# Performance work log

Hardware: AMD Instinct MI355X
Metric: run time of the kernel (lower is better)

Reference implementation:

```python
import jax, jax.numpy as jnp
import numpy as np

HIDDEN = 256
NUM_REL = 6
NUM_BASES = 30
N_NODES = 50000
N_EDGES = 800000


def rgcn_gate_layer(x, src, dst, etype, basis, att, root, bias, gate_w, gate_b):
    # Basis-decomposed relation weights: W_r = sum_b att[r,b] * basis[b]
    N = x.shape[0]
    W = jnp.einsum('rb,bio->rio', att, basis)           # [R, d, d]
    # Transform all nodes under every relation (cheaper than per-edge matmul
    # since N*R < E), then gather the per-edge message.
    xw = jnp.einsum('nd,rde->rne', x, W)                # [R, N, d]
    msg = xw[etype, src]                                # [E, d]
    # Scalar sigmoid gate per edge message
    g = jax.nn.sigmoid(msg @ gate_w + gate_b)           # [E, 1]
    gated = g * msg
    # Mean aggregation over incoming edges per destination node
    agg = jax.ops.segment_sum(gated, dst, num_segments=N)
    deg = jax.ops.segment_sum(jnp.ones((src.shape[0], 1), x.dtype), dst,
                              num_segments=N)
    agg = agg / jnp.maximum(deg, 1.0)
    return agg + x @ root + bias


def setup_inputs() -> dict:
    key = jax.random.key(0)
    ks = jax.random.split(key, 16)
    d = HIDDEN
    inp = {
        'x': jax.random.normal(ks[0], (N_NODES, d), jnp.float32),
        'edge_src': jax.random.randint(ks[1], (N_EDGES,), 0, N_NODES, jnp.int32),
        'edge_dst': jax.random.randint(ks[2], (N_EDGES,), 0, N_NODES, jnp.int32),
        'edge_type': jax.random.randint(ks[3], (N_EDGES,), 0, NUM_REL, jnp.int32),
    }
    def glorot(k, shape):
        fan = shape[-2] + shape[-1]
        return jax.random.uniform(k, shape, jnp.float32,
                                  -np.sqrt(6.0 / fan), np.sqrt(6.0 / fan))
    for li, off in ((1, 4), (2, 10)):
        inp[f'basis{li}'] = glorot(ks[off + 0], (NUM_BASES, d, d))
        inp[f'att{li}'] = glorot(ks[off + 1], (NUM_REL, NUM_BASES))
        inp[f'root{li}'] = glorot(ks[off + 2], (d, d))
        inp[f'bias{li}'] = jnp.zeros((d,), jnp.float32)
        inp[f'gate_w{li}'] = glorot(ks[off + 3], (d, 1))
        inp[f'gate_b{li}'] = jnp.zeros((1,), jnp.float32)
    return inp


def reference(x, edge_src, edge_dst, edge_type,
              basis1, att1, root1, bias1, gate_w1, gate_b1,
              basis2, att2, root2, bias2, gate_w2, gate_b2):
    h = jax.nn.relu(rgcn_gate_layer(x, edge_src, edge_dst, edge_type,
                                    basis1, att1, root1, bias1,
                                    gate_w1, gate_b1))
    out = rgcn_gate_layer(h, edge_src, edge_dst, edge_type,
                          basis2, att2, root2, bias2, gate_w2, gate_b2)
    return out
```

## Files before the change

kernel.cpp:

```cpp
#include <hip/hip_runtime.h>
#include <cmath>

#define HIDDEN 256
#define NUM_REL 6
#define KA 1536
#define KB 1792
#define NK64 28
#define NKA64 24
#define CTSTRIDE 28672

typedef float f32x4_t __attribute__((ext_vector_type(4)));
typedef short bf16x8_t __attribute__((ext_vector_type(8)));

__device__ __forceinline__ float bf2f(ushort u) {
  return __uint_as_float(((uint)u) << 16);
}
__device__ __forceinline__ ushort f2bf(float f) {
  uint u = __float_as_uint(f);
  u += 0x7FFFu + ((u >> 16) & 1u);
  return (ushort)(u >> 16);
}

__global__ __launch_bounds__(256) void prep_weights(
    const float* __restrict__ att, const float* __restrict__ basis,
    const float* __restrict__ root, const float* __restrict__ gw,
    ushort* __restrict__ BTf, float* __restrict__ gatevec) {
  const int d = blockIdx.x, r = blockIdx.y, o = threadIdx.x;
  float v;
  if (r < 6) {
    float s = 0.f;
#pragma unroll
    for (int b = 0; b < 30; ++b)
      s += att[r * 30 + b] * basis[(size_t)b * 65536 + d * 256 + o];
    v = s;
  } else {
    v = root[d * 256 + o];
  }
  const int gk = r * 256 + d;
  BTf[(size_t)(o >> 4) * CTSTRIDE + (gk >> 3) * 128 + (o & 15) * 8 +
      (gk & 7)] = f2bf(v);
  if (r < 6) {
    float t = v * gw[o];
#pragma unroll
    for (int off = 32; off; off >>= 1) t += __shfl_xor(t, off);
    __shared__ float sums[4];
    if ((o & 63) == 0) sums[o >> 6] = t;
    __syncthreads();
    if (o == 0) gatevec[r * 256 + d] = sums[0] + sums[1] + sums[2] + sums[3];
  }
}

__global__ __launch_bounds__(256) void gdot_kernel(
    const void* __restrict__ xin, int xIsF32, ushort* __restrict__ xbOut,
    const float* __restrict__ gatevec, const float* __restrict__ gate_b,
    float* __restrict__ G, int N) {
  const int wave = (blockIdx.x * blockDim.x + threadIdx.x) >> 6;
  if (wave >= N) return;
  const int l = threadIdx.x & 63;
  float x0, x1, x2, x3;
  if (xIsF32) {
    float4 xv = ((const float4*)xin)[(size_t)wave * 64 + l];
    x0 = xv.x; x1 = xv.y; x2 = xv.z; x3 = xv.w;
    ushort4 o;
    o.x = f2bf(x0); o.y = f2bf(x1); o.z = f2bf(x2); o.w = f2bf(x3);
    ((ushort4*)xbOut)[(size_t)wave * 64 + l] = o;
  } else {
    ushort4 xv = ((const ushort4*)xin)[(size_t)wave * 64 + l];
    x0 = bf2f(xv.x); x1 = bf2f(xv.y); x2 = bf2f(xv.z); x3 = bf2f(xv.w);
  }
  float out = 0.f;
#pragma unroll
  for (int r = 0; r < NUM_REL; ++r) {
    float4 gv = ((const float4*)(gatevec + r * 256))[l];
    float d = x0 * gv.x + x1 * gv.y + x2 * gv.z + x3 * gv.w;
#pragma unroll
    for (int off = 32; off; off >>= 1) d += __shfl_xor(d, off);
    if (l == r) out = d;
  }
  if (l < NUM_REL) {
    const float gb = gate_b[0];
    G[(size_t)l * N + wave] = 1.f / (1.f + __expf(-(out + gb)));
  }
}

#define ACCUM(rj, gj, vj)                                                  \
  do {                                                                    \
    const float fx = (gj)*bf2f((vj).x), fy = (gj)*bf2f((vj).y);           \
    const float fz = (gj)*bf2f((vj).z), fw = (gj)*bf2f((vj).w);           \
    switch (rj) {                                                         \
      case 0: a0x += fx; a0y += fy; a0z += fz; a0w += fw; break;          \
      case 1: a1x += fx; a1y += fy; a1z += fz; a1w += fw; break;          \
      case 2: a2x += fx; a2y += fy; a2z += fz; a2w += fw; break;          \
      case 3: a3x += fx; a3y += fy; a3z += fz; a3w += fw; break;          \
      case 4: a4x += fx; a4y += fy; a4z += fz; a4w += fw; break;          \
      default: a5x += fx; a5y += fy; a5z += fz; a5w += fw; break;         \
    }                                                                     \
  } while (0)

#define RELOF(ei) ((ei >= b1) + (ei >= b2) + (ei >= b3) + (ei >= b4) + (ei >= b5))

__global__ __launch_bounds__(256) void edge_agg(
    const ushort* __restrict__ xb, const float* __restrict__ G,
    const int* __restrict__ rp8, const int* __restrict__ src_s,
    ushort* __restrict__ A, int N) {
  const int n = (blockIdx.x * blockDim.x + threadIdx.x) >> 6;
  if (n >= N) return;
  const int l = threadIdx.x & 63;
  const int b0 = rp8[n * 8 + 0], b1 = rp8[n * 8 + 1], b2 = rp8[n * 8 + 2];
  const int b3 = rp8[n * 8 + 3], b4 = rp8[n * 8 + 4], b5 = rp8[n * 8 + 5];
  const int b6 = rp8[n * 8 + 6];

  float a0x = 0, a0y = 0, a0z = 0, a0w = 0, a1x = 0, a1y = 0, a1z = 0, a1w = 0;
  float a2x = 0, a2y = 0, a2z = 0, a2w = 0, a3x = 0, a3y = 0, a3z = 0, a3w = 0;
  float a4x = 0, a4y = 0, a4z = 0, a4w = 0, a5x = 0, a5y = 0, a5z = 0, a5w = 0;

  int e = b0;
  for (; e + 7 < b6; e += 8) {
    const int s0 = src_s[e + 0], s1 = src_s[e + 1];
    const int s2 = src_s[e + 2], s3 = src_s[e + 3];
    const int s4 = src_s[e + 4], s5 = src_s[e + 5];
    const int s6 = src_s[e + 6], s7 = src_s[e + 7];
    const ushort4 v0 = ((const ushort4*)(xb + (size_t)s0 * 256))[l];
    const ushort4 v1 = ((const ushort4*)(xb + (size_t)s1 * 256))[l];
    const ushort4 v2 = ((const ushort4*)(xb + (size_t)s2 * 256))[l];
    const ushort4 v3 = ((const ushort4*)(xb + (size_t)s3 * 256))[l];
    const ushort4 v4 = ((const ushort4*)(xb + (size_t)s4 * 256))[l];
    const ushort4 v5 = ((const ushort4*)(xb + (size_t)s5 * 256))[l];
    const ushort4 v6 = ((const ushort4*)(xb + (size_t)s6 * 256))[l];
    const ushort4 v7 = ((const ushort4*)(xb + (size_t)s7 * 256))[l];
    const int r0 = RELOF(e + 0), r1 = RELOF(e + 1), r2 = RELOF(e + 2),
              r3 = RELOF(e + 3), r4 = RELOF(e + 4), r5 = RELOF(e + 5),
              r6 = RELOF(e + 6), r7 = RELOF(e + 7);
    const float g0 = G[(size_t)r0 * N + s0], g1 = G[(size_t)r1 * N + s1];
    const float g2 = G[(size_t)r2 * N + s2], g3 = G[(size_t)r3 * N + s3];
    const float g4 = G[(size_t)r4 * N + s4], g5 = G[(size_t)r5 * N + s5];
    const float g6 = G[(size_t)r6 * N + s6], g7 = G[(size_t)r7 * N + s7];
    ACCUM(r0, g0, v0); ACCUM(r1, g1, v1); ACCUM(r2, g2, v2); ACCUM(r3, g3, v3);
    ACCUM(r4, g4, v4); ACCUM(r5, g5, v5); ACCUM(r6, g6, v6); ACCUM(r7, g7, v7);
  }
  for (; e < b6; ++e) {
    const int s0 = src_s[e];
    const ushort4 v0 = ((const ushort4*)(xb + (size_t)s0 * 256))[l];
    const int r0 = RELOF(e);
    const float g0 = G[(size_t)r0 * N + s0];
    ACCUM(r0, g0, v0);
  }

  const float inv = 1.f / fmaxf((float)(b6 - b0), 1.f);
  ushort* Arow = A + (size_t)n * KA;
  ushort4 o;
  o.x = f2bf(a0x * inv); o.y = f2bf(a0y * inv); o.z = f2bf(a0z * inv); o.w = f2bf(a0w * inv);
  ((ushort4*)(Arow + 0 * 256))[l] = o;
  o.x = f2bf(a1x * inv); o.y = f2bf(a1y * inv); o.z = f2bf(a1z * inv); o.w = f2bf(a1w * inv);
  ((ushort4*)(Arow + 1 * 256))[l] = o;
  o.x = f2bf(a2x * inv); o.y = f2bf(a2y * inv); o.z = f2bf(a2z * inv); o.w = f2bf(a2w * inv);
  ((ushort4*)(Arow + 2 * 256))[l] = o;
  o.x = f2bf(a3x * inv); o.y = f2bf(a3y * inv); o.z = f2bf(a3z * inv); o.w = f2bf(a3w * inv);
  ((ushort4*)(Arow + 3 * 256))[l] = o;
  o.x = f2bf(a4x * inv); o.y = f2bf(a4y * inv); o.z = f2bf(a4z * inv); o.w = f2bf(a4w * inv);
  ((ushort4*)(Arow + 4 * 256))[l] = o;
  o.x = f2bf(a5x * inv); o.y = f2bf(a5y * inv); o.z = f2bf(a5z * inv); o.w = f2bf(a5w * inv);
  ((ushort4*)(Arow + 5 * 256))[l] = o;
}

__global__ __launch_bounds__(256) void gemm_fused(
    const ushort* __restrict__ A, const ushort* __restrict__ xb,
    const ushort* __restrict__ BTf, const float* __restrict__ bias,
    void* __restrict__ outPtr, int M, int mode) {
  __shared__ ushort As[3][64 * 64];
  const int row0 = blockIdx.x * 64;
  const int tid = threadIdx.x;
  const int w = tid >> 6, l = tid & 63;

  const int srow0 = tid >> 3;
  const int gc = (tid & 7) ^ (srow0 & 7);
  const int ga0 = min(row0 + srow0, M - 1);
  const int ga1 = min(row0 + 32 + srow0, M - 1);
  const ushort* gpA0 = A + (size_t)ga0 * KA + gc * 8;
  const ushort* gpA1 = A + (size_t)ga1 * KA + gc * 8;
  const ushort* gpX0 = xb + (size_t)ga0 * 256 + gc * 8;
  const ushort* gpX1 = xb + (size_t)ga1 * 256 + gc * 8;

  const ushort* Bb =
      BTf + (size_t)(w * 4) * CTSTRIDE + (l >> 4) * 128 + (l & 15) * 8;

  f32x4_t acc[4][4] = {};

  auto stage = [&](int k, int buf) {
    const int ko = k * 64;
    const ushort* g0 = (k < NKA64) ? (gpA0 + ko) : (gpX0 + (ko - KA));
    const ushort* g1 = (k < NKA64) ? (gpA1 + ko) : (gpX1 + (ko - KA));
    __builtin_amdgcn_global_load_lds(
        (const __attribute__((address_space(1))) void*)g0,
        (__attribute__((address_space(3))) void*)(&As[buf][(size_t)tid * 8]),
        16, 0, 0);
    __builtin_amdgcn_global_load_lds(
        (const __attribute__((address_space(1))) void*)g1,
        (__attribute__((address_space(3))) void*)(&As[buf][(size_t)(256 + tid) * 8]),
        16, 0, 0);
  };

  auto compute = [&](int buf, const bf16x8_t (*b)[4]) {
#pragma unroll
    for (int ks = 0; ks < 2; ++ks) {
      bf16x8_t a[4];
#pragma unroll
      for (int m = 0; m < 4; ++m) {
        const int rr = m * 16 + (l & 15);
        const int s = (ks * 4 + (l >> 4)) ^ (rr & 7);
        a[m] = *(const bf16x8_t*)(&As[buf][rr * 64 + s * 8]);
      }
#pragma unroll
      for (int m = 0; m < 4; ++m)
#pragma unroll
        for (int n = 0; n < 4; ++n)
          acc[m][n] = __builtin_amdgcn_mfma_f32_16x16x32_bf16(
              a[m], b[ks][n], acc[m][n], 0, 0, 0);
    }
  };

  bf16x8_t bE[2][4], bO[2][4];
  stage(0, 0);
  stage(1, 1);
#pragma unroll
  for (int ks = 0; ks < 2; ++ks)
#pragma unroll
    for (int n = 0; n < 4; ++n)
      bE[ks][n] = *(const bf16x8_t*)(Bb + (size_t)n * CTSTRIDE + ks * 512);

  for (int k = 0; k < NK64; k += 2) {
    asm volatile("s_waitcnt vmcnt(10)" ::: "memory");
    __builtin_amdgcn_s_barrier();
#pragma unroll
    for (int ks = 0; ks < 2; ++ks)
#pragma unroll
      for (int n = 0; n < 4; ++n)
        bO[ks][n] = *(const bf16x8_t*)(Bb + (size_t)n * CTSTRIDE +
                                       (size_t)(k + 1) * 1024 + ks * 512);
    if (k + 2 < NK64) stage(k + 2, (k + 2) % 3);
    compute(k % 3, bE);

    asm volatile("s_waitcnt vmcnt(10)" ::: "memory");
    __builtin_amdgcn_s_barrier();
    if (k + 2 < NK64) {
#pragma unroll
      for (int ks = 0; ks < 2; ++ks)
#pragma unroll
        for (int n = 0; n < 4; ++n)
          bE[ks][n] = *(const bf16x8_t*)(Bb + (size_t)n * CTSTRIDE +
                                         (size_t)(k + 2) * 1024 + ks * 512);
    }
    if (k + 3 < NK64) stage(k + 3, (k + 3) % 3);
    compute((k + 1) % 3, bO);
  }

  const int rbase = row0 + (l >> 4) * 4;
  const int cbase = w * 64 + (l & 15);
#pragma unroll
  for (int n = 0; n < 4; ++n) {
    const int col = cbase + n * 16;
    const float bv = bias[col];
#pragma unroll
    for (int m = 0; m < 4; ++m)
#pragma unroll
      for (int i = 0; i < 4; ++i) {
        const int row = rbase + m * 16 + i;
        if (row < M) {
          float v = acc[m][n][i] + bv;
          if (mode == 0) {
            v = fmaxf(v, 0.f);
            ((ushort*)outPtr)[(size_t)row * 256 + col] = f2bf(v);
          } else {
            ((float*)outPtr)[(size_t)row * 256 + col] = v;
          }
        }
      }
  }
}

__global__ void hist_kernel(const int* __restrict__ dst,
                            const int* __restrict__ ety,
                            int* __restrict__ cnt, int* __restrict__ erank,
                            int E) {
  int stride = gridDim.x * blockDim.x;
  for (int e = blockIdx.x * blockDim.x + threadIdx.x; e < E; e += stride)
    erank[e] = atomicAdd(&cnt[dst[e] * 8 + ety[e]], 1);
}

__global__ void scan_reduce(const int* __restrict__ cnt,
                            int* __restrict__ blockSums, int n) {
  __shared__ int sd[256];
  int base = blockIdx.x * 1024;
  int t = threadIdx.x;
  int s = 0;
#pragma unroll
  for (int i = 0; i < 4; ++i) {
    int idx = base + t * 4 + i;
    s += (idx < n) ? cnt[idx] : 0;
  }
  sd[t] = s; __syncthreads();
  for (int off = 128; off; off >>= 1) {
    if (t < off) sd[t] += sd[t + off];
    __syncthreads();
  }
  if (t == 0) blockSums[blockIdx.x] = sd[0];
}

__global__ void scan_offsets(int* __restrict__ blockSums, int nb) {
  __shared__ int sd[512];
  const int t = threadIdx.x;
  const int v = (t < nb) ? blockSums[t] : 0;
  sd[t] = v; __syncthreads();
  for (int off = 1; off < 512; off <<= 1) {
    int u = (t >= off) ? sd[t - off] : 0;
    __syncthreads();
    sd[t] += u;
    __syncthreads();
  }
  if (t < nb) blockSums[t] = sd[t] - v;
}

__global__ void scan_write(const int* __restrict__ cnt,
                           const int* __restrict__ blockSums,
                           int* __restrict__ row_ptr, int n) {
  __shared__ int sd[256];
  int base = blockIdx.x * 1024;
  int t = threadIdx.x;
  int v[4]; int s = 0;
#pragma unroll
  for (int i = 0; i < 4; ++i) {
    int idx = base + t * 4 + i;
    v[i] = (idx < n) ? cnt[idx] : 0;
    s += v[i];
  }
  sd[t] = s; __syncthreads();
  for (int off = 1; off < 256; off <<= 1) {
    int val = (t >= off) ? sd[t - off] : 0;
    __syncthreads();
    sd[t] += val;
    __syncthreads();
  }
  int excl = blockSums[blockIdx.x] + sd[t] - s;
  for (int i = 0; i < 4; ++i) {
    int idx = base + t * 4 + i;
    if (idx < n) {
      row_ptr[idx] = excl;
      excl += v[i];
      if (idx == n - 1) row_ptr[n] = excl;
    }
  }
}

__global__ void scatter_kernel(const int* __restrict__ src,
                               const int* __restrict__ dst,
                               const int* __restrict__ ety,
                               const int* __restrict__ row_ptr,
                               const int* __restrict__ erank,
                               int* __restrict__ src_s, int E) {
  int stride = gridDim.x * blockDim.x;
  for (int e = blockIdx.x * blockDim.x + threadIdx.x; e < E; e += stride) {
    int bin = dst[e] * 8 + ety[e];
    src_s[row_ptr[bin] + erank[e]] = src[e];
  }
}

static inline size_t align16(size_t x) { return (x + 15) & ~(size_t)15; }

extern "C" void kernel_launch(void* const* d_in, const int* in_sizes, int n_in,
                              void* d_out, int out_size, void* d_ws,
                              size_t ws_size, hipStream_t stream) {
  const float* x    = (const float*)d_in[0];
  const int*   src  = (const int*)d_in[1];
  const int*   dst  = (const int*)d_in[2];
  const int*   ety  = (const int*)d_in[3];

  const int N   = in_sizes[0] / HIDDEN;
  const int E   = in_sizes[1];
  const int RN2 = N * 8;

  char* p = (char*)d_ws;
  ushort* BTf    = (ushort*)p; p += align16(((size_t)16 * CTSTRIDE + 4096) * 2);
  float* gatevec = (float*)p;  p += align16((size_t)NUM_REL * 256 * 4);
  float* G       = (float*)p;  p += align16((size_t)NUM_REL * N * 4);
  ushort* xb0    = (ushort*)p; p += align16((size_t)N * HIDDEN * 2);
  ushort* xb1    = (ushort*)p; p += align16((size_t)N * HIDDEN * 2);
  int* cnt       = (int*)p;    p += align16((size_t)RN2 * 4);
  int* erank     = (int*)p;    p += align16((size_t)E * 4);
  int* row_ptr   = (int*)p;    p += align16((size_t)(RN2 + 1) * 4);
  int* blockSums = (int*)p;    p += 2048;
  int* src_s     = (int*)p;    p += align16((size_t)E * 4);
  ushort* A      = (ushort*)p;

  const int scanBlocks = (RN2 + 1023) / 1024;

  hipMemsetAsync(cnt, 0, (size_t)RN2 * sizeof(int), stream);
  hist_kernel<<<2048, 256, 0, stream>>>(dst, ety, cnt, erank, E);
  scan_reduce<<<scanBlocks, 256, 0, stream>>>(cnt, blockSums, RN2);
  scan_offsets<<<1, 512, 0, stream>>>(blockSums, scanBlocks);
  scan_write<<<scanBlocks, 256, 0, stream>>>(cnt, blockSums, row_ptr, RN2);
  scatter_kernel<<<2048, 256, 0, stream>>>(src, dst, ety, row_ptr, erank,
                                           src_s, E);

  const int nodeBlocks = (N * 64 + 255) / 256;
  const int gemmGrid = (N + 63) / 64;

  for (int layer = 0; layer < 2; ++layer) {
    const float* bas  = (const float*)d_in[layer ? 10 : 4];
    const float* att  = (const float*)d_in[layer ? 11 : 5];
    const float* root = (const float*)d_in[layer ? 12 : 6];
    const float* bias = (const float*)d_in[layer ? 13 : 7];
    const float* gw   = (const float*)d_in[layer ? 14 : 8];
    const float* gb   = (const float*)d_in[layer ? 15 : 9];
    const ushort* xb  = layer ? xb1 : xb0;
    void* outp = layer ? d_out : (void*)xb1;
    const int mode = layer ? 1 : 0;

    prep_weights<<<dim3(256, 7), 256, 0, stream>>>(att, bas, root, gw, BTf,
                                                   gatevec);
    gdot_kernel<<<nodeBlocks, 256, 0, stream>>>(
        layer ? (const void*)xb1 : (const void*)x, layer ? 0 : 1, xb0,
        gatevec, gb, G, N);
    edge_agg<<<nodeBlocks, 256, 0, stream>>>(xb, G, row_ptr, src_s, A, N);
    gemm_fused<<<gemmGrid, 256, 0, stream>>>(A, xb, BTf, bias, outp, N, mode);
  }
}
```

Measured before the change: 482.7 us.

## Process nodes in descending-degree order in edge aggregation for load balance

Adds a counting sort of nodes by in-degree (histogram, scan, scatter) and has edge_agg pick its node through this permutation, so high-degree nodes are scheduled first and wave work is more uniform. The scatter kernel also switches from a grid-stride loop to one thread per edge. Costs are three small extra kernels, an indirection load per wave, and less locality in the output writes to A and in row_ptr reads.

```diff
diff --git a/kernel.cpp b/kernel.cpp
--- a/kernel.cpp
+++ b/kernel.cpp
@@ -102,9 +102,10 @@
 __global__ __launch_bounds__(256) void edge_agg(
     const ushort* __restrict__ xb, const float* __restrict__ G,
     const int* __restrict__ rp8, const int* __restrict__ src_s,
-    ushort* __restrict__ A, int N) {
-  const int n = (blockIdx.x * blockDim.x + threadIdx.x) >> 6;
-  if (n >= N) return;
+    const int* __restrict__ perm, ushort* __restrict__ A, int N) {
+  const int wid = (blockIdx.x * blockDim.x + threadIdx.x) >> 6;
+  if (wid >= N) return;
+  const int n = perm[wid];
   const int l = threadIdx.x & 63;
   const int b0 = rp8[n * 8 + 0], b1 = rp8[n * 8 + 1], b2 = rp8[n * 8 + 2];
   const int b3 = rp8[n * 8 + 3], b4 = rp8[n * 8 + 4], b5 = rp8[n * 8 + 5];
@@ -357,11 +358,34 @@
                                const int* __restrict__ row_ptr,
                                const int* __restrict__ erank,
                                int* __restrict__ src_s, int E) {
-  int stride = gridDim.x * blockDim.x;
-  for (int e = blockIdx.x * blockDim.x + threadIdx.x; e < E; e += stride) {
-    int bin = dst[e] * 8 + ety[e];
-    src_s[row_ptr[bin] + erank[e]] = src[e];
-  }
+  int e = blockIdx.x * blockDim.x + threadIdx.x;
+  if (e >= E) return;
+  int bin = dst[e] * 8 + ety[e];
+  src_s[row_ptr[bin] + erank[e]] = src[e];
+}
+
+__global__ void deg_hist(const int* __restrict__ rp8, int* __restrict__ dcnt,
+                         int N) {
+  int n = blockIdx.x * blockDim.x + threadIdx.x;
+  if (n >= N) return;
+  int d = rp8[n * 8 + 6] - rp8[n * 8];
+  atomicAdd(&dcnt[63 - min(d, 63)], 1);
+}
+
+__global__ void deg_scan(const int* __restrict__ dcnt, int* __restrict__ dcur) {
+  if (threadIdx.x == 0) {
+    int run = 0;
+    for (int i = 0; i < 64; ++i) { dcur[i] = run; run += dcnt[i]; }
+  }
+}
+
+__global__ void deg_scatter(const int* __restrict__ rp8, int* __restrict__ dcur,
+                            int* __restrict__ perm, int N) {
+  int n = blockIdx.x * blockDim.x + threadIdx.x;
+  if (n >= N) return;
+  int d = rp8[n * 8 + 6] - rp8[n * 8];
+  int pos = atomicAdd(&dcur[63 - min(d, 63)], 1);
+  perm[pos] = n;
 }
 
 static inline size_t align16(size_t x) { return (x + 15) & ~(size_t)15; }
@@ -388,18 +412,27 @@
   int* erank     = (int*)p;    p += align16((size_t)E * 4);
   int* row_ptr   = (int*)p;    p += align16((size_t)(RN2 + 1) * 4);
   int* blockSums = (int*)p;    p += 2048;
+  int* dbuf      = (int*)p;    p += 1024;
+  int* perm      = (int*)p;    p += align16((size_t)N * 4);
   int* src_s     = (int*)p;    p += align16((size_t)E * 4);
   ushort* A      = (ushort*)p;
 
+  int* dcnt = dbuf;
+  int* dcur = dbuf + 64;
+
   const int scanBlocks = (RN2 + 1023) / 1024;
 
   hipMemsetAsync(cnt, 0, (size_t)RN2 * sizeof(int), stream);
+  hipMemsetAsync(dcnt, 0, 64 * sizeof(int), stream);
   hist_kernel<<<2048, 256, 0, stream>>>(dst, ety, cnt, erank, E);
   scan_reduce<<<scanBlocks, 256, 0, stream>>>(cnt, blockSums, RN2);
   scan_offsets<<<1, 512, 0, stream>>>(blockSums, scanBlocks);
   scan_write<<<scanBlocks, 256, 0, stream>>>(cnt, blockSums, row_ptr, RN2);
-  scatter_kernel<<<2048, 256, 0, stream>>>(src, dst, ety, row_ptr, erank,
-                                           src_s, E);
+  scatter_kernel<<<(E + 255) / 256, 256, 0, stream>>>(src, dst, ety, row_ptr,
+                                                      erank, src_s, E);
+  deg_hist<<<(N + 255) / 256, 256, 0, stream>>>(row_ptr, dcnt, N);
+  deg_scan<<<1, 64, 0, stream>>>(dcnt, dcur);
+  deg_scatter<<<(N + 255) / 256, 256, 0, stream>>>(row_ptr, dcur, perm, N);
 
   const int nodeBlocks = (N * 64 + 255) / 256;
   const int gemmGrid = (N + 63) / 64;
@@ -420,7 +453,8 @@
     gdot_kernel<<<nodeBlocks, 256, 0, stream>>>(
         layer ? (const void*)xb1 : (const void*)x, layer ? 0 : 1, xb0,
         gatevec, gb, G, N);
-    edge_agg<<<nodeBlocks, 256, 0, stream>>>(xb, G, row_ptr, src_s, A, N);
+    edge_agg<<<nodeBlocks, 256, 0, stream>>>(xb, G, row_ptr, src_s, perm, A,
+                                             N);
     gemm_fused<<<gemmGrid, 256, 0, stream>>>(A, xb, BTf, bias, outp, N, mode);
   }
 }
```

After: 784.5 us. 1.63x slower.
